# Kernel optimization log

Hardware: AMD Instinct MI355X
Metric: run time of the kernel (lower is better)

The kernel has to match this reference:

```python
import jax, jax.numpy as jnp
import numpy as np

N_GRAPHS = 512  # number of graphs in the batch
S2S_STEPS = 3   # Set2Set processing_steps


def segment_softmax(e, seg, num_seg):
    m = jax.ops.segment_max(e, seg, num_segments=num_seg)
    ex = jnp.exp(e - m[seg])
    s = jax.ops.segment_sum(ex, seg, num_segments=num_seg)
    return ex / s[seg]


def setup_inputs() -> dict:
    key = jax.random.key(0)
    ks = jax.random.split(key, 24)
    N, E, Fin, Fe, D = 30000, 480000, 25, 14, 256
    s = 0.05
    inp = {
        "x": jax.random.normal(ks[0], (N, Fin), jnp.float32),
        "edge_attr": jax.random.normal(ks[1], (E, Fe), jnp.float32),
        # lin0
        "W0": jax.random.normal(ks[2], (Fin, D), jnp.float32) * s,
        "b0": jnp.zeros((D,), jnp.float32),
        # DMPNN edge-message MLP: [x_src || e_attr] -> D -> D
        "Wm1": jax.random.normal(ks[3], (D + Fe, D), jnp.float32) * s,
        "bm1": jnp.zeros((D,), jnp.float32),
        "Wm2": jax.random.normal(ks[4], (D, D), jnp.float32) * s,
        "bm2": jnp.zeros((D,), jnp.float32),
        # node (root) update
        "Wr": jax.random.normal(ks[5], (D, D), jnp.float32) * s,
        "br": jnp.zeros((D,), jnp.float32),
        # Set2Set LSTM: input 2D -> hidden D
        "Wih": jax.random.normal(ks[6], (2 * D, 4 * D), jnp.float32) * s,
        "Whh": jax.random.normal(ks[7], (D, 4 * D), jnp.float32) * s,
        "bl": jnp.zeros((4 * D,), jnp.float32),
        # readout MLP
        "W1": jax.random.normal(ks[8], (2 * D, D), jnp.float32) * s,
        "b1": jnp.zeros((D,), jnp.float32),
        "W2": jax.random.normal(ks[9], (D, 1), jnp.float32) * s,
        "b2": jnp.zeros((1,), jnp.float32),
        "edge_index": jax.random.randint(ks[10], (2, E), 0, N, jnp.int32),
        "batch": jnp.sort(jax.random.randint(ks[11], (N,), 0, N_GRAPHS, jnp.int32)),
    }
    return inp


def reference(x, edge_attr, W0, b0, Wm1, bm1, Wm2, bm2, Wr, br,
              Wih, Whh, bl, W1, b1, W2, b2, edge_index, batch):
    N = x.shape[0]
    # lin0 + relu
    h0 = jax.nn.relu(x @ W0 + b0)  # [N, D]
    # DMPNNLayer2: edge-conditioned message, sum-aggregate, root update (eval: no dropout)
    src, dst = edge_index[0], edge_index[1]
    m = jax.nn.relu(jnp.concatenate([h0[src], edge_attr], axis=-1) @ Wm1 + bm1)  # [E, D]
    m = m @ Wm2 + bm2
    agg = jax.ops.segment_sum(m, dst, num_segments=N)  # [N, D]
    out = jax.nn.relu(h0 @ Wr + br + agg)  # relu in top-level forward, massage_depth=1
    # Set2Set pooling (processing_steps=3)
    D = out.shape[1]
    B = N_GRAPHS
    q_star = jnp.zeros((B, 2 * D), out.dtype)
    h = jnp.zeros((B, D), out.dtype)
    c = jnp.zeros((B, D), out.dtype)
    for _ in range(S2S_STEPS):
        gates = q_star @ Wih + h @ Whh + bl  # [B, 4D]
        i, f, g, o = jnp.split(gates, 4, axis=-1)
        c = jax.nn.sigmoid(f) * c + jax.nn.sigmoid(i) * jnp.tanh(g)
        h = jax.nn.sigmoid(o) * jnp.tanh(c)
        e = jnp.sum(out * h[batch], axis=-1)              # [N]
        a = segment_softmax(e, batch, B)                  # [N]
        r = jax.ops.segment_sum(a[:, None] * out, batch, num_segments=B)  # [B, D]
        q_star = jnp.concatenate([h, r], axis=-1)
    # readout (eval: dropout identity)
    y = jax.nn.relu(q_star @ W1 + b1)
    y = y @ W2 + b2
    return y.reshape(-1)
```

## Files before the change

### kernel.cpp

```cpp
#include <hip/hip_runtime.h>

typedef unsigned short u16;
typedef unsigned char u8;
typedef unsigned int u32;
using s16x8 = __attribute__((ext_vector_type(8))) short;
using s16x4 = __attribute__((ext_vector_type(4))) short;
using f32x4 = __attribute__((ext_vector_type(4))) float;

#define DEV static __device__ __forceinline__

DEV float b2f(u16 u) { return __uint_as_float(((u32)u) << 16); }
DEV u16 f2bu(float f) {
    u32 u = __float_as_uint(f);
    u32 r = (u + 0x7FFFu + ((u >> 16) & 1u)) >> 16;
    return (u16)r;
}
DEV float sigm(float x) { return 1.0f / (1.0f + expf(-x)); }

DEV float ldv(const void* p, int i, int f32flag) {
    if (f32flag) return ((const float*)p)[i];
    return b2f(((const u16*)p)[i]);
}
DEV void stv(void* p, int i, float v, int f32flag) {
    if (f32flag) ((float*)p)[i] = v;
    else ((u16*)p)[i] = f2bu(v);
}

DEV int lower_bound(const int* b, int n, int v) {
    int lo = 0, hi = n;
    while (lo < hi) { int mid = (lo + hi) >> 1; if (b[mid] < v) lo = mid + 1; else hi = mid; }
    return lo;
}

__global__ void DMPNN_Change_678604832935_kernel(int* p) {
    if (p && threadIdx.x == 0 && blockIdx.x == 0) p[0] = 1;
}

__global__ void detect_kernel(const void* x, int* flag) {
    __shared__ int cnt[128];
    int tid = threadIdx.x;
    if (tid < 128) {
        u16 v = ((const u16*)x)[tid];
        int e = (v >> 7) & 0xFF;
        cnt[tid] = (e >= 100 && e <= 141) ? 1 : 0;
    }
    __syncthreads();
    if (tid == 0) {
        int s = 0;
        for (int i = 0; i < 128; ++i) s += cnt[i];
        flag[0] = (s < 110) ? 1 : 0;
    }
}

__global__ void fillv_kernel(void* out, const int* flag, float v) {
    int i = blockIdx.x * 256 + threadIdx.x;
    if (i < 512) stv(out, i, v, flag[0]);
}

__global__ void zero_kernel(float* p, int n) {
    int i = blockIdx.x * 256 + threadIdx.x;
    int stride = gridDim.x * 256;
    for (; i < n; i += stride) p[i] = 0.0f;
}

__global__ void zero2_kernel(float* a, int na, float* b, int nb) {
    int i = blockIdx.x * 256 + threadIdx.x;
    int stride = gridDim.x * 256;
    for (int j = i; j < na; j += stride) a[j] = 0.0f;
    for (int j = i; j < nb; j += stride) b[j] = 0.0f;
}

__global__ void hist_kernel(const int* __restrict__ eidx, u32* __restrict__ cnt) {
    int i = blockIdx.x * 256 + threadIdx.x;
    if (i < 480000) atomicAdd(&cnt[eidx[480000 + i]], 1u);
}

__global__ void scan1_kernel(const u32* __restrict__ cnt, u32* __restrict__ part) {
    __shared__ u32 s[256];
    int i = blockIdx.x * 256 + threadIdx.x;
    s[threadIdx.x] = (i < 30000) ? cnt[i] : 0u;
    __syncthreads();
    for (int st = 128; st > 0; st >>= 1) {
        if (threadIdx.x < st) s[threadIdx.x] += s[threadIdx.x + st];
        __syncthreads();
    }
    if (threadIdx.x == 0) part[blockIdx.x] = s[0];
}

__global__ void scan2_kernel(const u32* __restrict__ part, u32* __restrict__ pexcl, int nb) {
    int tid = threadIdx.x;
    u32 v = (tid < nb) ? part[tid] : 0u;
    u32 x = v;
    #pragma unroll
    for (int off = 1; off < 64; off <<= 1) {
        u32 t = __shfl_up(x, off, 64);
        if ((tid & 63) >= off) x += t;
    }
    __shared__ u32 wsum;
    if (tid == 63) wsum = x;
    __syncthreads();
    u32 add = (tid >= 64) ? wsum : 0u;
    if (tid < nb) pexcl[tid] = x + add - v;
}

__global__ void scan3_kernel(u32* __restrict__ cursor, const u32* __restrict__ pexcl) {
    __shared__ u32 s[256];
    int b = blockIdx.x, tid = threadIdx.x;
    int i = b * 256 + tid;
    u32 v = (i < 30000) ? cursor[i] : 0u;
    s[tid] = v;
    __syncthreads();
    for (int off = 1; off < 256; off <<= 1) {
        u32 t = (tid >= off) ? s[tid - off] : 0u;
        __syncthreads();
        s[tid] += t;
        __syncthreads();
    }
    u32 excl = s[tid] - v + pexcl[b];
    if (i < 30000) cursor[i] = excl;
}

__global__ void scatter_kernel(const int* __restrict__ eidx, u32* __restrict__ cursor,
                               u16* __restrict__ permLo, u8* __restrict__ permHi) {
    int i = blockIdx.x * 256 + threadIdx.x;
    if (i < 480000) {
        int d = eidx[480000 + i];
        u32 pos = atomicAdd(&cursor[d], 1u);
        permLo[pos] = (u16)(i & 0xFFFF);
        permHi[pos] = (u8)(i >> 16);
    }
}

__global__ void deg_kernel(const u32* __restrict__ cursor, float* __restrict__ degf) {
    int i = blockIdx.x * 256 + threadIdx.x;
    if (i < 30000) {
        u32 end = cursor[i];
        u32 beg = (i > 0) ? cursor[i - 1] : 0u;
        degf[i] = (float)(end - beg);
    }
}

__global__ void to_blocked_all(const void* Wm1, const void* Wm2, const void* Wr,
                               const void* Wih, const void* Whh, const int* flag,
                               u16* Wm1b, u16* Wm2b, u16* Wrb, u16* Wcatb) {
    const int T1 = 9 * 4 * 256 * 8;
    const int T2 = T1 + 8 * 4 * 256 * 8;
    const int T3 = T2 + 8 * 4 * 256 * 8;
    const int T4 = T3 + 24 * 4 * 1024 * 8;
    int idx = blockIdx.x * 256 + threadIdx.x;
    if (idx >= T4) return;
    int f32 = flag[0];
    if (idx < T3) {
        const void* src; u16* dst; int K; int l;
        if (idx < T1)      { src = Wm1; dst = Wm1b; K = 270; l = idx; }
        else if (idx < T2) { src = Wm2; dst = Wm2b; K = 256; l = idx - T1; }
        else               { src = Wr;  dst = Wrb;  K = 256; l = idx - T2; }
        int c = l & 7;
        int n = (l >> 3) & 255;
        int jk = l >> 11;
        int j = jk & 3, kt = jk >> 2;
        int k = kt * 32 + j * 8 + c;
        u16 v = 0;
        if (k < K) v = f2bu(ldv(src, k * 256 + n, f32));
        dst[l] = v;
    } else {
        int l = idx - T3;
        int c = l & 7;
        int n = (l >> 3) & 1023;
        int jk = l >> 13;
        int j = jk & 3, kt = jk >> 2;
        int k = kt * 32 + j * 8 + c;
        u16 v = 0;
        if (k < 512) v = f2bu(ldv(Wih, k * 1024 + n, f32));
        else if (k < 768) v = f2bu(ldv(Whh, (k - 512) * 1024 + n, f32));
        Wcatb[l] = v;
    }
}

__global__ __launch_bounds__(256) void lin0_kernel(const void* x, const void* W0,
                                                   const void* b0, const int* flag,
                                                   u16* h0b) {
    int f32 = flag[0];
    int n0 = blockIdx.x * 8, tid = threadIdx.x;
    __shared__ float xs[8][26];
    if (tid < 200) {
        int nn = tid / 25, k = tid % 25;
        xs[nn][k] = ldv(x, (n0 + nn) * 25 + k, f32);
    }
    __syncthreads();
    float wr[25];
    #pragma unroll
    for (int k = 0; k < 25; ++k) wr[k] = ldv(W0, k * 256 + tid, f32);
    float bias = ldv(b0, tid, f32);
    #pragma unroll
    for (int nn = 0; nn < 8; ++nn) {
        float a = bias;
        #pragma unroll
        for (int k = 0; k < 25; ++k) a += xs[nn][k] * wr[k];
        h0b[(n0 + nn) * 256 + tid] = f2bu(fmaxf(a, 0.0f));
    }
}

__global__ __launch_bounds__(256) void qgen_kernel(
    const u16* __restrict__ h0b, const u16* __restrict__ Wm1b,
    u16* __restrict__ Qb) {
    __shared__ __attribute__((aligned(16))) u16 As[64 * 264];
    const int tid = threadIdx.x;
    const int w = tid >> 6, lane = tid & 63, quad = lane >> 4, mrow = lane & 15;
    const int row0 = blockIdx.x * 64;
    const int colb = w * 64 + mrow;
    const int r = tid >> 2, sub = tid & 3;

    {
        int row = row0 + r;
        u16* arow = As + r * 264;
        #pragma unroll
        for (int j = 0; j < 8; ++j) {
            int c0 = sub * 64 + j * 8;
            s16x8 v = {0, 0, 0, 0, 0, 0, 0, 0};
            if (row < 30000) v = *(const s16x8*)(h0b + row * 256 + c0);
            *(s16x8*)(arow + c0) = v;
        }
    }
    __syncthreads();

    f32x4 acc[4][4];
    f32x4 fzero = {0.f, 0.f, 0.f, 0.f};
    #pragma unroll
    for (int mi = 0; mi < 4; ++mi)
        #pragma unroll
        for (int ni = 0; ni < 4; ++ni) acc[mi][ni] = fzero;

    for (int kt = 0; kt < 8; ++kt) {
        s16x8 af[4], bf[4];
        #pragma unroll
        for (int ni = 0; ni < 4; ++ni)
            bf[ni] = *(const s16x8*)(Wm1b + (((kt * 4 + quad) * 256) + colb + ni * 16) * 8);
        #pragma unroll
        for (int mi = 0; mi < 4; ++mi)
            af[mi] = *(const s16x8*)(As + (mi * 16 + mrow) * 264 + kt * 32 + quad * 8);
        #pragma unroll
        for (int mi = 0; mi < 4; ++mi)
            #pragma unroll
            for (int ni = 0; ni < 4; ++ni)
                acc[mi][ni] = __builtin_amdgcn_mfma_f32_16x16x32_bf16(af[mi], bf[ni], acc[mi][ni], 0, 0, 0);
    }

    #pragma unroll
    for (int mi = 0; mi < 4; ++mi)
        #pragma unroll
        for (int rg = 0; rg < 4; ++rg) {
            int row = row0 + mi * 16 + quad * 4 + rg;
            if (row >= 30000) continue;
            #pragma unroll
            for (int ni = 0; ni < 4; ++ni)
                Qb[row * 256 + colb + ni * 16] = f2bu(acc[mi][ni][rg]);
        }
}

#define MAXD 96
__global__ __launch_bounds__(256) void edge_mfma_node_kernel(
    const u16* __restrict__ Qb, const void* __restrict__ eattr,
    const int* __restrict__ eidx,
    const u16* __restrict__ permLo, const u8* __restrict__ permHi,
    const u32* __restrict__ cursor,
    const u16* __restrict__ Wm1b, const void* __restrict__ bm1,
    const int* __restrict__ flag, float* __restrict__ aggP) {
    const int f32 = flag[0];
    const int n = blockIdx.x, tid = threadIdx.x;
    const int w = tid >> 6, lane = tid & 63, quad = lane >> 4, mrow = lane & 15;
    const int beg = (n > 0) ? (int)cursor[n - 1] : 0;
    const int end = (int)cursor[n];
    __shared__ int eids[MAXD];
    __shared__ int sorted_s[MAXD];
    __shared__ int srcs16[16];
    __shared__ __attribute__((aligned(16))) u16 Ae[16 * 40];

    const int colb = w * 64 + mrow;
    s16x8 bf[4];
    float bm1c[4];
    #pragma unroll
    for (int ni = 0; ni < 4; ++ni) {
        bf[ni] = *(const s16x8*)(Wm1b + (((32 + quad) * 256) + colb + ni * 16) * 8);
        bm1c[ni] = ldv(bm1, colb + ni * 16, f32);
    }

    float psum[4] = {0.f, 0.f, 0.f, 0.f};
    const f32x4 fzero = {0.f, 0.f, 0.f, 0.f};

    for (int base = beg; base < end; base += MAXD) {
        int wcnt = end - base; if (wcnt > MAXD) wcnt = MAXD;
        if (tid < wcnt) {
            int si = base + tid;
            eids[tid] = (int)permLo[si] | ((int)permHi[si] << 16);
        }
        __syncthreads();
        if (tid < wcnt) {
            int key = eids[tid], r2 = 0;
            for (int j = 0; j < wcnt; ++j) r2 += (eids[j] < key);
            sorted_s[r2] = key;
        }
        __syncthreads();

        for (int cb = 0; cb < wcnt; cb += 16) {
            {
                int row = tid >> 4, c = tid & 15;
                int gi = cb + row;
                int e = (gi < wcnt) ? sorted_s[gi] : -1;
                u16 v = 0;
                if (e >= 0 && c < 14) v = f2bu(ldv(eattr, e * 14 + c, f32));
                Ae[row * 40 + c] = v;
                Ae[row * 40 + 16 + c] = 0;
                if (c == 0) srcs16[row] = (e >= 0) ? eidx[e] : 0;
            }
            __syncthreads();

            s16x8 af = *(const s16x8*)(Ae + mrow * 40 + quad * 8);
            f32x4 acc[4];
            #pragma unroll
            for (int ni = 0; ni < 4; ++ni)
                acc[ni] = __builtin_amdgcn_mfma_f32_16x16x32_bf16(af, bf[ni], fzero, 0, 0, 0);

            #pragma unroll
            for (int rg = 0; rg < 4; ++rg) {
                int row = quad * 4 + rg;
                if (cb + row < wcnt) {
                    const u16* qrow = Qb + srcs16[row] * 256;
                    #pragma unroll
                    for (int ni = 0; ni < 4; ++ni) {
                        float q = b2f(qrow[colb + ni * 16]);
                        psum[ni] += fmaxf(acc[ni][rg] + bm1c[ni] + q, 0.0f);
                    }
                }
            }
            __syncthreads();
        }
    }

    #pragma unroll
    for (int ni = 0; ni < 4; ++ni) {
        float v = psum[ni];
        v += __shfl_xor(v, 16, 64);
        v += __shfl_xor(v, 32, 64);
        psum[ni] = v;
    }
    if (quad == 0) {
        #pragma unroll
        for (int ni = 0; ni < 4; ++ni)
            aggP[n * 256 + colb + ni * 16] = psum[ni];
    }
}

__global__ __launch_bounds__(256) void edge_sorted_kernel(
    const u16* __restrict__ h0b, const void* __restrict__ eattr,
    const int* __restrict__ eidx,
    const u16* __restrict__ permLo, const u8* __restrict__ permHi,
    const u16* __restrict__ Wm1b,
    const void* __restrict__ bm1,
    const int* __restrict__ flag, float* __restrict__ aggP) {
    __shared__ __attribute__((aligned(16))) u16 As[64 * 296];
    __shared__ int dsh[64];
    const int f32 = flag[0];
    const int tid = threadIdx.x;
    const int w = tid >> 6, lane = tid & 63, quad = lane >> 4, mrow = lane & 15;
    const int eb0 = blockIdx.x * 64;
    const int colb = w * 64 + mrow;

    if (tid < 64) {
        int sj = eb0 + tid;
        int ee = (int)permLo[sj] | ((int)permHi[sj] << 16);
        dsh[tid] = eidx[480000 + ee];
    }
    {
        int r = tid >> 2, sub = tid & 3;
        int si = eb0 + r;
        int e = (int)permLo[si] | ((int)permHi[si] << 16);
        int src = eidx[e];
        const u16* hrow = h0b + src * 256;
        u16* arow = As + r * 296;
        #pragma unroll
        for (int j = 0; j < 8; ++j) {
            int c0 = sub * 64 + j * 8;
            *(s16x8*)(arow + c0) = *(const s16x8*)(hrow + c0);
        }
        if (sub == 0) {
            for (int c = 0; c < 14; ++c) arow[256 + c] = f2bu(ldv(eattr, e * 14 + c, f32));
            for (int c = 14; c < 40; ++c) arow[256 + c] = 0;
        }
    }
    __syncthreads();

    f32x4 acc[4][4];
    f32x4 fzero = {0.f, 0.f, 0.f, 0.f};
    #pragma unroll
    for (int mi = 0; mi < 4; ++mi)
        #pragma unroll
        for (int ni = 0; ni < 4; ++ni) acc[mi][ni] = fzero;

    for (int kt = 0; kt < 9; ++kt) {
        s16x8 af[4], bf[4];
        #pragma unroll
        for (int ni = 0; ni < 4; ++ni)
            bf[ni] = *(const s16x8*)(Wm1b + (((kt * 4 + quad) * 256) + colb + ni * 16) * 8);
        #pragma unroll
        for (int mi = 0; mi < 4; ++mi)
            af[mi] = *(const s16x8*)(As + (mi * 16 + mrow) * 296 + kt * 32 + quad * 8);
        #pragma unroll
        for (int mi = 0; mi < 4; ++mi)
            #pragma unroll
            for (int ni = 0; ni < 4; ++ni)
                acc[mi][ni] = __builtin_amdgcn_mfma_f32_16x16x32_bf16(af[mi], bf[ni], acc[mi][ni], 0, 0, 0);
    }

    float bm1c[4];
    #pragma unroll
    for (int ni = 0; ni < 4; ++ni) bm1c[ni] = ldv(bm1, colb + ni * 16, f32);
    __syncthreads();
    #pragma unroll
    for (int mi = 0; mi < 4; ++mi)
        #pragma unroll
        for (int ni = 0; ni < 4; ++ni)
            #pragma unroll
            for (int rg = 0; rg < 4; ++rg) {
                int row = mi * 16 + quad * 4 + rg;
                As[row * 296 + colb + ni * 16] = f2bu(fmaxf(acc[mi][ni][rg] + bm1c[ni], 0.0f));
            }
    __syncthreads();

    {
        int c = tid;
        float s = 0.0f;
        int cur = dsh[0];
        #pragma unroll 8
        for (int rr = 0; rr < 64; ++rr) {
            int d = dsh[rr];
            if (d != cur) { atomicAdd(&aggP[cur * 256 + c], s); s = 0.0f; cur = d; }
            s += b2f(As[rr * 296 + c]);
        }
        atomicAdd(&aggP[cur * 256 + c], s);
    }
}

__global__ __launch_bounds__(256) void node_dual_kernel(
    u16* __restrict__ h0b, const u16* __restrict__ Wrb, const u16* __restrict__ Wm2b,
    const void* __restrict__ br, const void* __restrict__ bm2,
    const float* __restrict__ aggP, const float* __restrict__ degf,
    const int* __restrict__ flag) {
    __shared__ __attribute__((aligned(16))) u16 As[64 * 264];
    const int f32 = flag[0];
    const int tid = threadIdx.x;
    const int w = tid >> 6, lane = tid & 63, quad = lane >> 4, mrow = lane & 15;
    const int row0 = blockIdx.x * 64;
    const int colb = w * 64 + mrow;
    const int r = tid >> 2, sub = tid & 3;

    {
        int row = row0 + r;
        u16* arow = As + r * 264;
        #pragma unroll
        for (int j = 0; j < 8; ++j) {
            int c0 = sub * 64 + j * 8;
            s16x8 v = {0, 0, 0, 0, 0, 0, 0, 0};
            if (row < 30000) v = *(const s16x8*)(h0b + row * 256 + c0);
            *(s16x8*)(arow + c0) = v;
        }
    }
    __syncthreads();

    f32x4 acc[4][4];
    f32x4 fzero = {0.f, 0.f, 0.f, 0.f};
    #pragma unroll
    for (int mi = 0; mi < 4; ++mi)
        #pragma unroll
        for (int ni = 0; ni < 4; ++ni) acc[mi][ni] = fzero;

    for (int kt = 0; kt < 8; ++kt) {
        s16x8 af[4], bf[4];
        #pragma unroll
        for (int ni = 0; ni < 4; ++ni)
            bf[ni] = *(const s16x8*)(Wrb + (((kt * 4 + quad) * 256) + colb + ni * 16) * 8);
        #pragma unroll
        for (int mi = 0; mi < 4; ++mi)
            af[mi] = *(const s16x8*)(As + (mi * 16 + mrow) * 264 + kt * 32 + quad * 8);
        #pragma unroll
        for (int mi = 0; mi < 4; ++mi)
            #pragma unroll
            for (int ni = 0; ni < 4; ++ni)
                acc[mi][ni] = __builtin_amdgcn_mfma_f32_16x16x32_bf16(af[mi], bf[ni], acc[mi][ni], 0, 0, 0);
    }
    __syncthreads();

    {
        int row = row0 + r;
        u16* arow = As + r * 264;
        #pragma unroll
        for (int j = 0; j < 8; ++j) {
            int c0 = sub * 64 + j * 8;
            s16x8 pk = {0, 0, 0, 0, 0, 0, 0, 0};
            if (row < 30000) {
                f32x4 a = *(const f32x4*)(aggP + row * 256 + c0);
                f32x4 b = *(const f32x4*)(aggP + row * 256 + c0 + 4);
                pk[0] = (short)f2bu(a[0]); pk[1] = (short)f2bu(a[1]);
                pk[2] = (short)f2bu(a[2]); pk[3] = (short)f2bu(a[3]);
                pk[4] = (short)f2bu(b[0]); pk[5] = (short)f2bu(b[1]);
                pk[6] = (short)f2bu(b[2]); pk[7] = (short)f2bu(b[3]);
            }
            *(s16x8*)(arow + c0) = pk;
        }
    }
    __syncthreads();

    for (int kt = 0; kt < 8; ++kt) {
        s16x8 af[4], bf[4];
        #pragma unroll
        for (int ni = 0; ni < 4; ++ni)
            bf[ni] = *(const s16x8*)(Wm2b + (((kt * 4 + quad) * 256) + colb + ni * 16) * 8);
        #pragma unroll
        for (int mi = 0; mi < 4; ++mi)
            af[mi] = *(const s16x8*)(As + (mi * 16 + mrow) * 264 + kt * 32 + quad * 8);
        #pragma unroll
        for (int mi = 0; mi < 4; ++mi)
            #pragma unroll
            for (int ni = 0; ni < 4; ++ni)
                acc[mi][ni] = __builtin_amdgcn_mfma_f32_16x16x32_bf16(af[mi], bf[ni], acc[mi][ni], 0, 0, 0);
    }

    #pragma unroll
    for (int mi = 0; mi < 4; ++mi)
        #pragma unroll
        for (int rg = 0; rg < 4; ++rg) {
            int row = row0 + mi * 16 + quad * 4 + rg;
            if (row >= 30000) continue;
            float dg = degf[row];
            #pragma unroll
            for (int ni = 0; ni < 4; ++ni) {
                int col = colb + ni * 16;
                float v = acc[mi][ni][rg] + ldv(br, col, f32) + dg * ldv(bm2, col, f32);
                h0b[row * 256 + col] = f2bu(fmaxf(v, 0.0f));
            }
        }
}

__global__ __launch_bounds__(256) void gates_mfma_kernel(
    const u16* __restrict__ Abuf, const u16* __restrict__ Wcatb,
    float* __restrict__ G) {
    const int tid = threadIdx.x;
    const int w = tid >> 6, lane = tid & 63, quad = lane >> 4, mrow = lane & 15;
    const int row0 = blockIdx.x * 64;
    const int col = blockIdx.y * 64 + w * 16 + mrow;

    f32x4 acc[4];
    f32x4 fzero = {0.f, 0.f, 0.f, 0.f};
    #pragma unroll
    for (int mi = 0; mi < 4; ++mi) acc[mi] = fzero;

    for (int kt = 0; kt < 24; ++kt) {
        s16x8 bfv = *(const s16x8*)(Wcatb + (((kt * 4 + quad) * 1024) + col) * 8);
        s16x8 af[4];
        #pragma unroll
        for (int mi = 0; mi < 4; ++mi)
            af[mi] = *(const s16x8*)(Abuf + (row0 + mi * 16 + mrow) * 768 + kt * 32 + quad * 8);
        #pragma unroll
        for (int mi = 0; mi < 4; ++mi)
            acc[mi] = __builtin_amdgcn_mfma_f32_16x16x32_bf16(af[mi], bfv, acc[mi], 0, 0, 0);
    }

    #pragma unroll
    for (int mi = 0; mi < 4; ++mi)
        #pragma unroll
        for (int rg = 0; rg < 4; ++rg)
            G[(row0 + mi * 16 + quad * 4 + rg) * 1024 + col] = acc[mi][rg];
}

#define GROWS 112
__global__ __launch_bounds__(256) void s2s_lstm_fused_kernel(
    const float* __restrict__ G, const void* __restrict__ bl,
    const int* __restrict__ flag, float* __restrict__ Cst, float* __restrict__ Hst,
    const u16* __restrict__ outb, const int* __restrict__ batch,
    float* __restrict__ Rst, u16* __restrict__ Abuf, float* __restrict__ ebuf) {
    __shared__ __attribute__((aligned(16))) u16 Ls[GROWS * 256];
    __shared__ __attribute__((aligned(16))) float hsh[256];
    __shared__ float esh[GROWS];
    __shared__ float red[256];
    const int b = blockIdx.x, tid = threadIdx.x;
    const int w = tid >> 6, lane = tid & 63;
    const int f32 = flag[0];

    {
        float gi = G[b * 1024 + tid]       + ldv(bl, tid, f32);
        float gf = G[b * 1024 + 256 + tid] + ldv(bl, 256 + tid, f32);
        float gg = G[b * 1024 + 512 + tid] + ldv(bl, 512 + tid, f32);
        float go = G[b * 1024 + 768 + tid] + ldv(bl, 768 + tid, f32);
        float c = Cst[b * 256 + tid];
        c = sigm(gf) * c + sigm(gi) * tanhf(gg);
        Cst[b * 256 + tid] = c;
        float h = sigm(go) * tanhf(c);
        Hst[b * 256 + tid] = h;
        u16 hb = f2bu(h);
        Abuf[b * 768 + tid] = hb;
        Abuf[b * 768 + 512 + tid] = hb;
        hsh[tid] = h;
    }
    const int n0 = lower_bound(batch, 30000, b);
    const int n1 = lower_bound(batch, 30000, b + 1);
    const int cnt = n1 - n0;
    __syncthreads();
    float r_out = 0.0f;
    if (cnt > 0 && cnt <= GROWS) {
        for (int idx = tid; idx < cnt * 32; idx += 256) {
            int i = idx >> 5, c8 = idx & 31;
            *(s16x8*)(Ls + i * 256 + c8 * 8) = *(const s16x8*)(outb + (n0 + i) * 256 + c8 * 8);
        }
        __syncthreads();
        for (int i = w; i < cnt; i += 4) {
            s16x4 ov = *(const s16x4*)(Ls + i * 256 + lane * 4);
            f32x4 hv = *(const f32x4*)(hsh + lane * 4);
            float p = b2f((u16)ov[0]) * hv[0] + b2f((u16)ov[1]) * hv[1]
                    + b2f((u16)ov[2]) * hv[2] + b2f((u16)ov[3]) * hv[3];
            #pragma unroll
            for (int off = 1; off < 64; off <<= 1) p += __shfl_xor(p, off, 64);
            if (lane == 0) esh[i] = p;
        }
        __syncthreads();
        float m = -1e30f;
        for (int i = tid; i < cnt; i += 256) m = fmaxf(m, esh[i]);
        red[tid] = m; __syncthreads();
        for (int s = 128; s > 0; s >>= 1) { if (tid < s) red[tid] = fmaxf(red[tid], red[tid + s]); __syncthreads(); }
        m = red[0]; __syncthreads();
        float sl = 0.0f;
        for (int i = tid; i < cnt; i += 256) { float pe = expf(esh[i] - m); esh[i] = pe; sl += pe; }
        red[tid] = sl; __syncthreads();
        for (int s = 128; s > 0; s >>= 1) { if (tid < s) red[tid] += red[tid + s]; __syncthreads(); }
        float ssum = red[0]; __syncthreads();
        float acc = 0.0f;
        for (int i = 0; i < cnt; ++i) acc += esh[i] * b2f(Ls[i * 256 + tid]);
        r_out = acc / ssum;
    } else if (cnt > GROWS) {
        for (int i = w; i < cnt; i += 4) {
            const u16* orow = outb + (n0 + i) * 256 + lane * 4;
            f32x4 hv = *(const f32x4*)(hsh + lane * 4);
            float p = b2f(orow[0]) * hv[0] + b2f(orow[1]) * hv[1]
                    + b2f(orow[2]) * hv[2] + b2f(orow[3]) * hv[3];
            #pragma unroll
            for (int off = 1; off < 64; off <<= 1) p += __shfl_xor(p, off, 64);
            if (lane == 0) ebuf[n0 + i] = p;
        }
        __syncthreads();
        float m = -1e30f;
        for (int n = n0 + tid; n < n1; n += 256) m = fmaxf(m, ebuf[n]);
        red[tid] = m; __syncthreads();
        for (int s = 128; s > 0; s >>= 1) { if (tid < s) red[tid] = fmaxf(red[tid], red[tid + s]); __syncthreads(); }
        m = red[0]; __syncthreads();
        float sl = 0.0f;
        for (int n = n0 + tid; n < n1; n += 256) sl += expf(ebuf[n] - m);
        red[tid] = sl; __syncthreads();
        for (int s = 128; s > 0; s >>= 1) { if (tid < s) red[tid] += red[tid + s]; __syncthreads(); }
        float ssum = red[0]; __syncthreads();
        float acc = 0.0f;
        for (int c0 = n0; c0 < n1; c0 += 256) {
            int nn = n1 - c0; if (nn > 256) nn = 256;
            __syncthreads();
            if (tid < nn) red[tid] = expf(ebuf[c0 + tid] - m);
            __syncthreads();
            for (int i = 0; i < nn; ++i) acc += red[i] * b2f(outb[(c0 + i) * 256 + tid]);
        }
        r_out = acc / ssum;
    }
    Rst[b * 256 + tid] = r_out;
    Abuf[b * 768 + 256 + tid] = f2bu(r_out);
}

__global__ __launch_bounds__(256) void readout_kernel(const float* Hst, const float* Rst,
                                                      const void* W1, const void* b1,
                                                      const void* W2, const void* b2,
                                                      const u16* nodeout, const float* aggP,
                                                      const int* flag, void* out) {
    int f32 = flag[0];
    int b = blockIdx.x, tid = threadIdx.x;
    __shared__ float qs[512];
    __shared__ float red[256];
    qs[tid] = Hst[b * 256 + tid];
    qs[256 + tid] = Rst[b * 256 + tid];
    __syncthreads();
    float a = ldv(b1, tid, f32);
    for (int k = 0; k < 512; ++k) a += qs[k] * ldv(W1, k * 256 + tid, f32);
    a = fmaxf(a, 0.0f) * ldv(W2, tid, f32);
    red[tid] = a; __syncthreads();
    for (int s = 128; s > 0; s >>= 1) { if (tid < s) red[tid] += red[tid + s]; __syncthreads(); }
    if (tid == 0) {
        float D = 0.0f;
        if (b == 0) {
            float s1 = 0.0f, s2 = 0.0f, s3 = 0.0f;
            for (int i = 0; i < 256; ++i) {
                s1 += fabsf(b2f(nodeout[i]));
                s2 += fabsf(aggP[i]);
                s3 += fabsf(Rst[i]);
            }
            if (s1 < 1e-3f) D += 100.0f;
            if (s2 < 1e-3f) D += 200.0f;
            if (s3 < 1e-6f) D += 400.0f;
        }
        stv(out, b, red[0] + ldv(b2, 0, f32) + D, f32);
    }
}

#define OFF_FLAG 0
#define OFF_HST  64
#define OFF_RST  524352
#define OFF_CST  1048640
#define OFF_PLO  64
#define OFF_PHI  960064
#define OFF_CUR  1440064
#define OFF_WREG 1572928
#define OFF_WM1B (OFF_WREG)
#define OFF_WM2B (OFF_WREG + 147456)
#define OFF_WRB  (OFF_WREG + 278528)
#define OFF_WCAT (OFF_WREG + 409600)
#define OFF_E    3670080
#define OFF_AGG  3790144
#define OFF_ABUF (OFF_AGG + 1048576)
#define OFF_G    (OFF_AGG + 4194304)
#define OFF_H0B  34510144
#define WS_NEEDED 49870144
#define OFF_Q    49870144
#define WS_FAST  (49870144 + 15360000)

extern "C" __attribute__((visibility("default")))
void kernel_launch(void* const* d_in, const int* in_sizes, int n_in,
                   void* d_out, int out_size, void* d_ws, size_t ws_size,
                   hipStream_t stream) {
    char* ws = (char*)d_ws;
    int*   flag   = (int*)(ws + OFF_FLAG);
    float* Hst    = (float*)(ws + OFF_HST);
    float* Rst    = (float*)(ws + OFF_RST);
    float* Cst    = (float*)(ws + OFF_CST);
    u16*   permLo = (u16*)(ws + OFF_PLO);
    u8*    permHi = (u8*)(ws + OFF_PHI);
    u32*   cursor = (u32*)(ws + OFF_CUR);
    u16*   Wm1b   = (u16*)(ws + OFF_WM1B);
    u16*   Wm2b   = (u16*)(ws + OFF_WM2B);
    u16*   Wrb    = (u16*)(ws + OFF_WRB);
    u16*   Wcatb  = (u16*)(ws + OFF_WCAT);
    float* ebuf   = (float*)(ws + OFF_E);
    u32*   part   = (u32*)(ws + OFF_E);
    u32*   pexcl  = (u32*)(ws + OFF_E + 512);
    float* degf   = (float*)(ws + OFF_E);
    float* aggP   = (float*)(ws + OFF_AGG);
    u16*   Abuf   = (u16*)(ws + OFF_ABUF);
    float* G      = (float*)(ws + OFF_G);
    u16*   h0b    = (u16*)(ws + OFF_H0B);
    u16*   Qb     = (u16*)(ws + OFF_Q);

    detect_kernel<<<1, 256, 0, stream>>>(d_in[0], flag);

    bool sizes_ok = (n_in == 19)
        && in_sizes[0] == 30000 * 25
        && in_sizes[1] == 480000 * 14
        && in_sizes[4] == 270 * 256
        && in_sizes[10] == 512 * 1024
        && in_sizes[17] == 2 * 480000
        && in_sizes[18] == 30000;
    if (!sizes_ok) { fillv_kernel<<<2, 256, 0, stream>>>(d_out, flag, 1600.0f); return; }
    if (ws_size < (size_t)WS_NEEDED) { fillv_kernel<<<2, 256, 0, stream>>>(d_out, flag, 800.0f); return; }
    const bool fast = (ws_size >= (size_t)WS_FAST);

    fillv_kernel<<<2, 256, 0, stream>>>(d_out, flag, 3.0f);
    DMPNN_Change_678604832935_kernel<<<1, 64, 0, stream>>>((int*)(ws + OFF_G));

    const void* x     = d_in[0];
    const void* eattr = d_in[1];
    const void* W0    = d_in[2];
    const void* b0    = d_in[3];
    const void* Wm1   = d_in[4];
    const void* bm1   = d_in[5];
    const void* Wm2   = d_in[6];
    const void* bm2   = d_in[7];
    const void* Wr    = d_in[8];
    const void* br    = d_in[9];
    const void* Wih   = d_in[10];
    const void* Whh   = d_in[11];
    const void* bl    = d_in[12];
    const void* W1    = d_in[13];
    const void* b1    = d_in[14];
    const void* W2    = d_in[15];
    const void* b2    = d_in[16];
    const int* eidx   = (const int*)d_in[17];
    const int* batch  = (const int*)d_in[18];

    to_blocked_all<<<3872, 256, 0, stream>>>(Wm1, Wm2, Wr, Wih, Whh, flag,
                                             Wm1b, Wm2b, Wrb, Wcatb);

    lin0_kernel<<<3750, 256, 0, stream>>>(x, W0, b0, flag, h0b);

    zero_kernel<<<30, 256, 0, stream>>>((float*)cursor, 30000);
    hist_kernel<<<1875, 256, 0, stream>>>(eidx, cursor);
    scan1_kernel<<<118, 256, 0, stream>>>(cursor, part);
    scan2_kernel<<<1, 128, 0, stream>>>(part, pexcl, 118);
    scan3_kernel<<<118, 256, 0, stream>>>(cursor, pexcl);
    scatter_kernel<<<1875, 256, 0, stream>>>(eidx, cursor, permLo, permHi);
    deg_kernel<<<118, 256, 0, stream>>>(cursor, degf);

    if (fast) {
        qgen_kernel<<<469, 256, 0, stream>>>(h0b, Wm1b, Qb);
        edge_mfma_node_kernel<<<30000, 256, 0, stream>>>(Qb, eattr, eidx, permLo, permHi,
                                                         cursor, Wm1b, bm1, flag, aggP);
    } else {
        zero_kernel<<<1024, 256, 0, stream>>>(aggP, 7680000);
        edge_sorted_kernel<<<7500, 256, 0, stream>>>(h0b, eattr, eidx, permLo, permHi,
                                                     Wm1b, bm1, flag, aggP);
    }
    node_dual_kernel<<<469, 256, 0, stream>>>(h0b, Wrb, Wm2b, br, bm2, aggP, degf, flag);

    zero2_kernel<<<256, 256, 0, stream>>>(Cst, 131072, (float*)Abuf, 196608);

    for (int s = 0; s < 3; ++s) {
        gates_mfma_kernel<<<dim3(8, 16), 256, 0, stream>>>(Abuf, Wcatb, G);
        s2s_lstm_fused_kernel<<<512, 256, 0, stream>>>(G, bl, flag, Cst, Hst,
                                                       h0b, batch, Rst, Abuf, ebuf);
    }
    readout_kernel<<<512, 256, 0, stream>>>(Hst, Rst, W1, b1, W2, b2, h0b, aggP, flag, d_out);
}
```

Before: 489.0 us.

## Fuse lin0 with Q projection and streamline per-node edge aggregation

Merges lin0 with the h0·Wm1 projection (qgen) into one kernel, so h0 is built in shared memory and Q is produced without re-reading h0. The scatter step now writes a compact 16-bit source-node array, which lets a new per-node edge kernel skip reading edge_index. That kernel reduces its partial sums with wave shuffles and writes the aggregate once in bf16 instead of using float atomics. The degree kernel is removed and degree is derived from the cursor inside node_dual. The risks are a larger workspace requirement, lower-precision aggregate storage, and a fallback path when the workspace is too small.

```diff
diff --git a/kernel.cpp b/kernel.cpp
--- a/kernel.cpp
+++ b/kernel.cpp
@@ -121,22 +121,15 @@
 }
 
 __global__ void scatter_kernel(const int* __restrict__ eidx, u32* __restrict__ cursor,
-                               u16* __restrict__ permLo, u8* __restrict__ permHi) {
+                               u16* __restrict__ permLo, u8* __restrict__ permHi,
+                               u16* __restrict__ srcW) {
     int i = blockIdx.x * 256 + threadIdx.x;
     if (i < 480000) {
         int d = eidx[480000 + i];
         u32 pos = atomicAdd(&cursor[d], 1u);
         permLo[pos] = (u16)(i & 0xFFFF);
         permHi[pos] = (u8)(i >> 16);
-    }
-}
-
-__global__ void deg_kernel(const u32* __restrict__ cursor, float* __restrict__ degf) {
-    int i = blockIdx.x * 256 + threadIdx.x;
-    if (i < 30000) {
-        u32 end = cursor[i];
-        u32 beg = (i > 0) ? cursor[i - 1] : 0u;
-        degf[i] = (float)(end - beg);
+        if (srcW) srcW[pos] = (u16)eidx[i];
     }
 }
 
@@ -201,6 +194,72 @@
     }
 }
 
+__global__ __launch_bounds__(256) void lin0q_kernel(
+    const void* x, const void* W0, const void* b0, const int* flag,
+    const u16* __restrict__ Wm1b, u16* __restrict__ h0b, u16* __restrict__ Qb) {
+    __shared__ __attribute__((aligned(16))) u16 As[64 * 264];
+    __shared__ float xs[64][26];
+    const int f32 = flag[0];
+    const int tid = threadIdx.x;
+    const int w = tid >> 6, lane = tid & 63, quad = lane >> 4, mrow = lane & 15;
+    const int row0 = blockIdx.x * 64;
+    const int colb = w * 64 + mrow;
+
+    for (int idx = tid; idx < 64 * 25; idx += 256) {
+        int i = idx / 25, k = idx - i * 25;
+        int row = row0 + i;
+        xs[i][k] = (row < 30000) ? ldv(x, row * 25 + k, f32) : 0.0f;
+    }
+    float wr[25];
+    #pragma unroll
+    for (int k = 0; k < 25; ++k) wr[k] = ldv(W0, k * 256 + tid, f32);
+    float bias = ldv(b0, tid, f32);
+    __syncthreads();
+    for (int i = 0; i < 64; ++i) {
+        float a = bias;
+        #pragma unroll
+        for (int k = 0; k < 25; ++k) a += xs[i][k] * wr[k];
+        u16 hb = f2bu(fmaxf(a, 0.0f));
+        As[i * 264 + tid] = hb;
+        int row = row0 + i;
+        if (row < 30000) h0b[row * 256 + tid] = hb;
+    }
+    __syncthreads();
+
+    f32x4 acc[4][4];
+    f32x4 fzero = {0.f, 0.f, 0.f, 0.f};
+    #pragma unroll
+    for (int mi = 0; mi < 4; ++mi)
+        #pragma unroll
+        for (int ni = 0; ni < 4; ++ni) acc[mi][ni] = fzero;
+
+    for (int kt = 0; kt < 8; ++kt) {
+        s16x8 af[4], bf[4];
+        #pragma unroll
+        for (int ni = 0; ni < 4; ++ni)
+            bf[ni] = *(const s16x8*)(Wm1b + (((kt * 4 + quad) * 256) + colb + ni * 16) * 8);
+        #pragma unroll
+        for (int mi = 0; mi < 4; ++mi)
+            af[mi] = *(const s16x8*)(As + (mi * 16 + mrow) * 264 + kt * 32 + quad * 8);
+        #pragma unroll
+        for (int mi = 0; mi < 4; ++mi)
+            #pragma unroll
+            for (int ni = 0; ni < 4; ++ni)
+                acc[mi][ni] = __builtin_amdgcn_mfma_f32_16x16x32_bf16(af[mi], bf[ni], acc[mi][ni], 0, 0, 0);
+    }
+
+    #pragma unroll
+    for (int mi = 0; mi < 4; ++mi)
+        #pragma unroll
+        for (int rg = 0; rg < 4; ++rg) {
+            int row = row0 + mi * 16 + quad * 4 + rg;
+            if (row >= 30000) continue;
+            #pragma unroll
+            for (int ni = 0; ni < 4; ++ni)
+                Qb[row * 256 + colb + ni * 16] = f2bu(acc[mi][ni][rg]);
+        }
+}
+
 __global__ __launch_bounds__(256) void qgen_kernel(
     const u16* __restrict__ h0b, const u16* __restrict__ Wm1b,
     u16* __restrict__ Qb) {
@@ -259,6 +318,107 @@
 }
 
 #define MAXD 96
+__global__ __launch_bounds__(256) void edge_mfma_node2_kernel(
+    const u16* __restrict__ Qb, const void* __restrict__ eattr,
+    const u16* __restrict__ srcW,
+    const u16* __restrict__ permLo, const u8* __restrict__ permHi,
+    const u32* __restrict__ cursor,
+    const u16* __restrict__ Wm1b, const void* __restrict__ bm1,
+    const int* __restrict__ flag, u16* __restrict__ aggB) {
+    const int f32 = flag[0];
+    const int n = blockIdx.x, tid = threadIdx.x;
+    const int w = tid >> 6, lane = tid & 63, quad = lane >> 4, mrow = lane & 15;
+    const int beg = (n > 0) ? (int)cursor[n - 1] : 0;
+    const int end = (int)cursor[n];
+    __shared__ int eids[MAXD];
+    __shared__ int srcl[MAXD];
+    __shared__ int sorted_s[MAXD];
+    __shared__ int sortedSrc[MAXD];
+    __shared__ __attribute__((aligned(16))) u16 Ae[16 * 40];
+
+    const int colb = w * 64 + mrow;
+    s16x8 bf[4];
+    float bm1c[4];
+    #pragma unroll
+    for (int ni = 0; ni < 4; ++ni) {
+        bf[ni] = *(const s16x8*)(Wm1b + (((32 + quad) * 256) + colb + ni * 16) * 8);
+        bm1c[ni] = ldv(bm1, colb + ni * 16, f32);
+    }
+
+    float psum[4] = {0.f, 0.f, 0.f, 0.f};
+    const f32x4 fzero = {0.f, 0.f, 0.f, 0.f};
+
+    for (int base = beg; base < end; base += MAXD) {
+        int wcnt = end - base; if (wcnt > MAXD) wcnt = MAXD;
+        if (tid < wcnt) {
+            int si = base + tid;
+            eids[tid] = (int)permLo[si] | ((int)permHi[si] << 16);
+            srcl[tid] = (int)srcW[si];
+        }
+        __syncthreads();
+        if (tid < wcnt) {
+            int key = eids[tid], r2 = 0;
+            for (int j = 0; j < wcnt; ++j) r2 += (eids[j] < key);
+            sorted_s[r2] = key;
+            sortedSrc[r2] = srcl[tid];
+        }
+        __syncthreads();
+
+        for (int cb = 0; cb < wcnt; cb += 16) {
+            {
+                int row = tid >> 4, c = tid & 15;
+                int gi = cb + row;
+                int e = (gi < wcnt) ? sorted_s[gi] : -1;
+                u16 v = 0;
+                if (e >= 0 && c < 14) v = f2bu(ldv(eattr, e * 14 + c, f32));
+                Ae[row * 40 + c] = v;
+                Ae[row * 40 + 16 + c] = 0;
+            }
+            __syncthreads();
+
+            float qv[4][4];
+            #pragma unroll
+            for (int rg = 0; rg < 4; ++rg) {
+                int gi = cb + quad * 4 + rg;
+                int sidx = (gi < wcnt) ? sortedSrc[gi] : 0;
+                const u16* qrow = Qb + sidx * 256;
+                #pragma unroll
+                for (int ni = 0; ni < 4; ++ni)
+                    qv[rg][ni] = b2f(qrow[colb + ni * 16]);
+            }
+
+            s16x8 af = *(const s16x8*)(Ae + mrow * 40 + quad * 8);
+            f32x4 acc[4];
+            #pragma unroll
+            for (int ni = 0; ni < 4; ++ni)
+                acc[ni] = __builtin_amdgcn_mfma_f32_16x16x32_bf16(af, bf[ni], fzero, 0, 0, 0);
+
+            #pragma unroll
+            for (int rg = 0; rg < 4; ++rg) {
+                if (cb + quad * 4 + rg < wcnt) {
+                    #pragma unroll
+                    for (int ni = 0; ni < 4; ++ni)
+                        psum[ni] += fmaxf(acc[ni][rg] + bm1c[ni] + qv[rg][ni], 0.0f);
+                }
+            }
+            __syncthreads();
+        }
+    }
+
+    #pragma unroll
+    for (int ni = 0; ni < 4; ++ni) {
+        float v = psum[ni];
+        v += __shfl_xor(v, 16, 64);
+        v += __shfl_xor(v, 32, 64);
+        psum[ni] = v;
+    }
+    if (quad == 0) {
+        #pragma unroll
+        for (int ni = 0; ni < 4; ++ni)
+            aggB[n * 256 + colb + ni * 16] = f2bu(psum[ni]);
+    }
+}
+
 __global__ __launch_bounds__(256) void edge_mfma_node_kernel(
     const u16* __restrict__ Qb, const void* __restrict__ eattr,
     const int* __restrict__ eidx,
@@ -444,7 +604,8 @@
 __global__ __launch_bounds__(256) void node_dual_kernel(
     u16* __restrict__ h0b, const u16* __restrict__ Wrb, const u16* __restrict__ Wm2b,
     const void* __restrict__ br, const void* __restrict__ bm2,
-    const float* __restrict__ aggP, const float* __restrict__ degf,
+    const void* __restrict__ aggV, int agg_bf16,
+    const u32* __restrict__ cursor,
     const int* __restrict__ flag) {
     __shared__ __attribute__((aligned(16))) u16 As[64 * 264];
     const int f32 = flag[0];
@@ -493,19 +654,31 @@
     {
         int row = row0 + r;
         u16* arow = As + r * 264;
-        #pragma unroll
-        for (int j = 0; j < 8; ++j) {
-            int c0 = sub * 64 + j * 8;
-            s16x8 pk = {0, 0, 0, 0, 0, 0, 0, 0};
-            if (row < 30000) {
-                f32x4 a = *(const f32x4*)(aggP + row * 256 + c0);
-                f32x4 b = *(const f32x4*)(aggP + row * 256 + c0 + 4);
-                pk[0] = (short)f2bu(a[0]); pk[1] = (short)f2bu(a[1]);
-                pk[2] = (short)f2bu(a[2]); pk[3] = (short)f2bu(a[3]);
-                pk[4] = (short)f2bu(b[0]); pk[5] = (short)f2bu(b[1]);
-                pk[6] = (short)f2bu(b[2]); pk[7] = (short)f2bu(b[3]);
+        if (agg_bf16) {
+            const u16* aggB = (const u16*)aggV;
+            #pragma unroll
+            for (int j = 0; j < 8; ++j) {
+                int c0 = sub * 64 + j * 8;
+                s16x8 v = {0, 0, 0, 0, 0, 0, 0, 0};
+                if (row < 30000) v = *(const s16x8*)(aggB + row * 256 + c0);
+                *(s16x8*)(arow + c0) = v;
             }
-            *(s16x8*)(arow + c0) = pk;
+        } else {
+            const float* aggP = (const float*)aggV;
+            #pragma unroll
+            for (int j = 0; j < 8; ++j) {
+                int c0 = sub * 64 + j * 8;
+                s16x8 pk = {0, 0, 0, 0, 0, 0, 0, 0};
+                if (row < 30000) {
+                    f32x4 a = *(const f32x4*)(aggP + row * 256 + c0);
+                    f32x4 b = *(const f32x4*)(aggP + row * 256 + c0 + 4);
+                    pk[0] = (short)f2bu(a[0]); pk[1] = (short)f2bu(a[1]);
+                    pk[2] = (short)f2bu(a[2]); pk[3] = (short)f2bu(a[3]);
+                    pk[4] = (short)f2bu(b[0]); pk[5] = (short)f2bu(b[1]);
+                    pk[6] = (short)f2bu(b[2]); pk[7] = (short)f2bu(b[3]);
+                }
+                *(s16x8*)(arow + c0) = pk;
+            }
         }
     }
     __syncthreads();
@@ -531,7 +704,7 @@
         for (int rg = 0; rg < 4; ++rg) {
             int row = row0 + mi * 16 + quad * 4 + rg;
             if (row >= 30000) continue;
-            float dg = degf[row];
+            float dg = (float)(cursor[row] - (row > 0 ? cursor[row - 1] : 0u));
             #pragma unroll
             for (int ni = 0; ni < 4; ++ni) {
                 int col = colb + ni * 16;
@@ -673,7 +846,8 @@
 __global__ __launch_bounds__(256) void readout_kernel(const float* Hst, const float* Rst,
                                                       const void* W1, const void* b1,
                                                       const void* W2, const void* b2,
-                                                      const u16* nodeout, const float* aggP,
+                                                      const u16* nodeout, const void* aggV,
+                                                      int agg_bf16,
                                                       const int* flag, void* out) {
     int f32 = flag[0];
     int b = blockIdx.x, tid = threadIdx.x;
@@ -693,7 +867,8 @@
             float s1 = 0.0f, s2 = 0.0f, s3 = 0.0f;
             for (int i = 0; i < 256; ++i) {
                 s1 += fabsf(b2f(nodeout[i]));
-                s2 += fabsf(aggP[i]);
+                s2 += agg_bf16 ? fabsf(b2f(((const u16*)aggV)[i]))
+                               : fabsf(((const float*)aggV)[i]);
                 s3 += fabsf(Rst[i]);
             }
             if (s1 < 1e-3f) D += 100.0f;
@@ -724,6 +899,8 @@
 #define WS_NEEDED 49870144
 #define OFF_Q    49870144
 #define WS_FAST  (49870144 + 15360000)
+#define OFF_SRC  (OFF_Q + 15360000)
+#define WS_FAST2 (OFF_SRC + 960000)
 
 extern "C" __attribute__((visibility("default")))
 void kernel_launch(void* const* d_in, const int* in_sizes, int n_in,
@@ -744,12 +921,12 @@
     float* ebuf   = (float*)(ws + OFF_E);
     u32*   part   = (u32*)(ws + OFF_E);
     u32*   pexcl  = (u32*)(ws + OFF_E + 512);
-    float* degf   = (float*)(ws + OFF_E);
     float* aggP   = (float*)(ws + OFF_AGG);
     u16*   Abuf   = (u16*)(ws + OFF_ABUF);
     float* G      = (float*)(ws + OFF_G);
     u16*   h0b    = (u16*)(ws + OFF_H0B);
     u16*   Qb     = (u16*)(ws + OFF_Q);
+    u16*   srcW   = (u16*)(ws + OFF_SRC);
 
     detect_kernel<<<1, 256, 0, stream>>>(d_in[0], flag);
 
@@ -762,7 +939,8 @@
         && in_sizes[18] == 30000;
     if (!sizes_ok) { fillv_kernel<<<2, 256, 0, stream>>>(d_out, flag, 1600.0f); return; }
     if (ws_size < (size_t)WS_NEEDED) { fillv_kernel<<<2, 256, 0, stream>>>(d_out, flag, 800.0f); return; }
-    const bool fast = (ws_size >= (size_t)WS_FAST);
+    const int fastlvl = (ws_size >= (size_t)WS_FAST2) ? 2
+                      : (ws_size >= (size_t)WS_FAST)  ? 1 : 0;
 
     fillv_kernel<<<2, 256, 0, stream>>>(d_out, flag, 3.0f);
     DMPNN_Change_678604832935_kernel<<<1, 64, 0, stream>>>((int*)(ws + OFF_G));
@@ -790,18 +968,27 @@
     to_blocked_all<<<3872, 256, 0, stream>>>(Wm1, Wm2, Wr, Wih, Whh, flag,
                                              Wm1b, Wm2b, Wrb, Wcatb);
 
-    lin0_kernel<<<3750, 256, 0, stream>>>(x, W0, b0, flag, h0b);
+    if (fastlvl >= 1) {
+        lin0q_kernel<<<469, 256, 0, stream>>>(x, W0, b0, flag, Wm1b, h0b, Qb);
+    } else {
+        lin0_kernel<<<3750, 256, 0, stream>>>(x, W0, b0, flag, h0b);
+    }
 
     zero_kernel<<<30, 256, 0, stream>>>((float*)cursor, 30000);
     hist_kernel<<<1875, 256, 0, stream>>>(eidx, cursor);
     scan1_kernel<<<118, 256, 0, stream>>>(cursor, part);
     scan2_kernel<<<1, 128, 0, stream>>>(part, pexcl, 118);
     scan3_kernel<<<118, 256, 0, stream>>>(cursor, pexcl);
-    scatter_kernel<<<1875, 256, 0, stream>>>(eidx, cursor, permLo, permHi);
-    deg_kernel<<<118, 256, 0, stream>>>(cursor, degf);
-
-    if (fast) {
-        qgen_kernel<<<469, 256, 0, stream>>>(h0b, Wm1b, Qb);
+    scatter_kernel<<<1875, 256, 0, stream>>>(eidx, cursor, permLo, permHi,
+                                             (fastlvl == 2) ? srcW : (u16*)nullptr);
+
+    int agg_bf16 = 0;
+    if (fastlvl == 2) {
+        agg_bf16 = 1;
+        edge_mfma_node2_kernel<<<30000, 256, 0, stream>>>(Qb, eattr, srcW, permLo, permHi,
+                                                          cursor, Wm1b, bm1, flag,
+                                                          (u16*)aggP);
+    } else if (fastlvl == 1) {
         edge_mfma_node_kernel<<<30000, 256, 0, stream>>>(Qb, eattr, eidx, permLo, permHi,
                                                          cursor, Wm1b, bm1, flag, aggP);
     } else {
@@ -809,7 +996,8 @@
         edge_sorted_kernel<<<7500, 256, 0, stream>>>(h0b, eattr, eidx, permLo, permHi,
                                                      Wm1b, bm1, flag, aggP);
     }
-    node_dual_kernel<<<469, 256, 0, stream>>>(h0b, Wrb, Wm2b, br, bm2, aggP, degf, flag);
+    node_dual_kernel<<<469, 256, 0, stream>>>(h0b, Wrb, Wm2b, br, bm2,
+                                              aggP, agg_bf16, cursor, flag);
 
     zero2_kernel<<<256, 256, 0, stream>>>(Cst, 131072, (float*)Abuf, 196608);
 
@@ -818,5 +1006,6 @@
         s2s_lstm_fused_kernel<<<512, 256, 0, stream>>>(G, bl, flag, Cst, Hst,
                                                        h0b, batch, Rst, Abuf, ebuf);
     }
-    readout_kernel<<<512, 256, 0, stream>>>(Hst, Rst, W1, b1, W2, b2, h0b, aggP, flag, d_out);
-}
+    readout_kernel<<<512, 256, 0, stream>>>(Hst, Rst, W1, b1, W2, b2, h0b,
+                                            aggP, agg_bf16, flag, d_out);
+}
```

Result: faster. 477.4 us (-2.4%).
